# Optimization experiments

Measured on AMD Instinct MI355X. Metric: run time of the kernel, lower is better.

Reference implementation:

```python
import jax, jax.numpy as jnp
import numpy as np
from jax import lax

B, D_MODEL, T = 4, 256, 8192
D_STATE, D_CONV = 16, 4
D_INNER = 2 * D_MODEL          # expand=2.0
DT_RANK = (D_MODEL + 15) // 16 # ceil(d_model/16) = 16
EPS = 1e-5


def setup_inputs() -> dict:
    key = jax.random.key(0)
    ks = jax.random.split(key, 12)
    s = lambda k, shape, scale=0.02: (jax.random.normal(k, shape, jnp.float32) * scale)
    x = jax.random.normal(ks[0], (B, D_MODEL, T), jnp.float32)
    ln_w = jnp.ones((D_MODEL,), jnp.float32)
    ln_b = jnp.zeros((D_MODEL,), jnp.float32)
    in_proj_w = s(ks[1], (2 * D_INNER, D_MODEL))
    conv_w = s(ks[2], (D_INNER, 1, D_CONV), 0.1)
    conv_b = jnp.zeros((D_INNER,), jnp.float32)
    x_proj_w = s(ks[3], (DT_RANK + 2 * D_STATE, D_INNER))
    dt_proj_w = s(ks[4], (D_INNER, DT_RANK), 0.1)
    # bias init so softplus(dt_bias) ~ small positive dt, like mamba_ssm
    dt_proj_b = jnp.log(jnp.expm1(jax.random.uniform(ks[5], (D_INNER,), jnp.float32, 0.001, 0.1)))
    # S4D-real init: A_log = log(1..d_state) broadcast over d_inner
    A_log = jnp.log(jnp.tile(jnp.arange(1, D_STATE + 1, dtype=jnp.float32), (D_INNER, 1)))
    D = jnp.ones((D_INNER,), jnp.float32)
    out_proj_w = s(ks[6], (D_MODEL, D_INNER))
    return {"x": x, "ln_w": ln_w, "ln_b": ln_b, "in_proj_w": in_proj_w,
            "conv_w": conv_w, "conv_b": conv_b, "x_proj_w": x_proj_w,
            "dt_proj_w": dt_proj_w, "dt_proj_b": dt_proj_b, "A_log": A_log,
            "D": D, "out_proj_w": out_proj_w}


def _mamba_block(x, ln_w, ln_b, in_proj_w, conv_w, conv_b, x_proj_w,
                 dt_proj_w, dt_proj_b, A_log, D, out_proj_w):
    # x: (B, C, T)
    residual = x
    xt = jnp.transpose(x, (0, 2, 1))  # (B, T, C)
    # channel layernorm
    mu = jnp.mean(xt, axis=-1, keepdims=True)
    var = jnp.var(xt, axis=-1, keepdims=True)
    xn = (xt - mu) * lax.rsqrt(var + EPS) * ln_w + ln_b
    # in_proj -> x, z
    xz = jnp.einsum('btc,ec->bte', xn, in_proj_w)  # (B,T,2*d_inner)
    x_in, z = jnp.split(xz, 2, axis=-1)
    # causal depthwise conv over time
    xc = jnp.transpose(x_in, (0, 2, 1))  # (B, d_inner, T)
    xc = lax.conv_general_dilated(xc, conv_w, window_strides=(1,),
                                  padding=[(D_CONV - 1, 0)],
                                  dimension_numbers=('NCH', 'OIH', 'NCH'),
                                  feature_group_count=D_INNER)
    xc = xc + conv_b[None, :, None]
    u = jax.nn.silu(jnp.transpose(xc, (0, 2, 1)))  # (B,T,d_inner)
    # x_proj -> dt, B, C
    dbl = jnp.einsum('btd,ed->bte', u, x_proj_w)
    dt, Bm, Cm = jnp.split(dbl, [DT_RANK, DT_RANK + D_STATE], axis=-1)
    delta = jax.nn.softplus(jnp.einsum('btr,dr->btd', dt, dt_proj_w) + dt_proj_b)  # (B,T,d_inner)
    A = -jnp.exp(A_log)  # (d_inner, d_state)
    deltaA = jnp.exp(jnp.einsum('btd,dn->btdn', delta, A))          # (B,T,d,n)
    deltaBu = jnp.einsum('btd,btn->btdn', delta * u, Bm)            # (B,T,d,n)
    # selective scan over time
    def step(h, inp):
        dA_t, dBu_t, C_t = inp
        h = dA_t * h + dBu_t                       # (B,d,n)
        y = jnp.einsum('bdn,bn->bd', h, C_t)
        return h, y
    h0 = jnp.zeros((x.shape[0], D_INNER, D_STATE), x.dtype)
    _, ys = lax.scan(step, h0, (jnp.moveaxis(deltaA, 1, 0),
                                jnp.moveaxis(deltaBu, 1, 0),
                                jnp.moveaxis(Cm, 1, 0)))
    y = jnp.moveaxis(ys, 0, 1) + u * D             # (B,T,d_inner)
    y = y * jax.nn.silu(z)
    out = jnp.einsum('btd,cd->btc', y, out_proj_w)  # (B,T,C)
    return jnp.transpose(out, (0, 2, 1)) + residual


def reference(x, ln_w, ln_b, in_proj_w, conv_w, conv_b, x_proj_w,
              dt_proj_w, dt_proj_b, A_log, D, out_proj_w):
    return _mamba_block(x, ln_w, ln_b, in_proj_w, conv_w, conv_b, x_proj_w,
                        dt_proj_w, dt_proj_b, A_log, D, out_proj_w)
```

## Files before the change

### kernel.cpp

```cpp
#include <hip/hip_runtime.h>

typedef unsigned short u16;
typedef unsigned int u32;
typedef __bf16 bfx8 __attribute__((ext_vector_type(8)));
typedef float f32x4 __attribute__((ext_vector_type(4)));

#define Tn 8192
#define Bn 4
#define MTOT 32768
#define CH 128
#define TC 64

#define OFF_W     0ul
#define OFF_AL2   917504ul
#define OFF_XN    (1ul<<20)
#define OFF_XIN   (17ul<<20)
#define OFF_Z     (49ul<<20)
#define OFF_U     (81ul<<20)
#define OFF_DBLDT (113ul<<20)
#define OFF_BCF   (115ul<<20)
#define OFF_DELTA (119ul<<20)
#define OFF_P     (151ul<<20)
#define OFF_CC    (167ul<<20)

__device__ __forceinline__ float b2f(u16 h){ return __uint_as_float(((u32)h)<<16); }
__device__ __forceinline__ u16 f2b(float f){
  u32 u = __float_as_uint(f);
  return (u16)((u + 0x7FFFu + ((u>>16)&1u)) >> 16);
}
__device__ __forceinline__ float aexp2(float x){ float r; asm("v_exp_f32 %0, %1" : "=v"(r) : "v"(x)); return r; }
__device__ __forceinline__ float arcp (float x){ float r; asm("v_rcp_f32 %0, %1" : "=v"(r) : "v"(x)); return r; }
__device__ __forceinline__ float alog2(float x){ float r; asm("v_log_f32 %0, %1" : "=v"(r) : "v"(x)); return r; }
__device__ __forceinline__ float fsilu(float a){ return a*arcp(1.f + aexp2(-a*1.44269504f)); }
__device__ __forceinline__ float fsoftplus(float v){
  float r = 0.69314718f*alog2(1.f + aexp2(v*1.44269504f));
  return (v > 20.f) ? v : r;
}
typedef const __attribute__((address_space(1))) void* gp1_t;
typedef __attribute__((address_space(3))) void* lp3_t;
__device__ __forceinline__ void gload_lds16(const void* g, void* l){
  __builtin_amdgcn_global_load_lds((gp1_t)g, (lp3_t)l, 16, 0, 0);
}

__global__ void wconv_k(const float* __restrict__ inw, const float* __restrict__ xpw,
                        const float* __restrict__ dtw, const float* __restrict__ opw,
                        const float* __restrict__ alog, u16* __restrict__ W, float* __restrict__ aL2)
{
  int i = blockIdx.x*256 + threadIdx.x;
  if (i < 262144) { W[i] = f2b(inw[i]); return; }
  if (i < 294912) { int j = i - 262144; int r = j >> 9, k = j & 511;
    float v = (r < 16) ? xpw[r*512 + k] : ((r < 32) ? 0.f : xpw[(r-16)*512 + k]);
    W[i] = f2b(v); return; }
  if (i < 311296) { int j = i - 294912; int d = j >> 5, k = j & 31;
    W[i] = f2b((k < 16) ? dtw[d*16 + k] : 0.f); return; }
  if (i < 442368) { W[i] = f2b(opw[i - 311296]); return; }
  if (i < 450560) { int j = i - 442368; aL2[j] = -__expf(alog[j]) * 1.44269504088896f; return; }
}

__global__ __launch_bounds__(256)
void ln_k(const float* __restrict__ x, const float* __restrict__ lnw,
          const float* __restrict__ lnb, u16* __restrict__ xn)
{
  const int t0 = blockIdx.x*64, b = blockIdx.y;
  const int tid = threadIdx.x, cg = tid>>6, tl = tid&63;
  __shared__ float ps[4][64], pq[4][64], mu[64], rs[64];
  float s = 0.f, q = 0.f;
  for (int ci = 0; ci < 64; ci++){
    int c = ci*4 + cg;
    float v = x[((size_t)(b*256 + c))*Tn + t0 + tl];
    s += v; q += v*v;
  }
  ps[cg][tl] = s; pq[cg][tl] = q;
  __syncthreads();
  if (tid < 64){
    float S = ps[0][tid]+ps[1][tid]+ps[2][tid]+ps[3][tid];
    float Q = pq[0][tid]+pq[1][tid]+pq[2][tid]+pq[3][tid];
    float m = S*(1.f/256.f);
    float var = Q*(1.f/256.f) - m*m;
    mu[tid] = m; rs[tid] = rsqrtf(var + 1e-5f);
  }
  __syncthreads();
  const float w = lnw[tid&255], bb = lnb[tid&255];
  for (int t = 0; t < 64; t++){
    float v = x[((size_t)(b*256 + tid))*Tn + t0 + t];
    xn[((size_t)(b*Tn) + t0 + t)*256 + tid] = f2b((v - mu[t])*rs[t]*w + bb);
  }
}

template<int BN, int EPI>
__global__ __launch_bounds__(256)
void gemm_k(const u16* __restrict__ A, int lda,
            const u16* __restrict__ Bw, int ldb,
            u16* __restrict__ O, u16* __restrict__ O2, float* __restrict__ Of, int ldo,
            const float* __restrict__ bias, int K)
{
  constexpr int NFR = BN/32;
  __shared__ __align__(16) u16 sA[128*32];
  __shared__ __align__(16) u16 sB[BN*32];
  const int tid = threadIdx.x;
  const int m0 = blockIdx.x*128, n0 = blockIdx.y*BN;
  const int lane = tid & 63, wid = tid >> 6;
  const int wr = wid >> 1, wc = wid & 1;
  const int lr = lane & 15, g = lane >> 4;
  const f32x4 fz = {0.f,0.f,0.f,0.f};
  f32x4 acc[4][NFR];
  #pragma unroll
  for (int m=0;m<4;m++)
    #pragma unroll
    for (int n=0;n<NFR;n++) acc[m][n] = fz;
  const int nk = K >> 5;
  for (int kt = 0; kt < nk; ++kt){
    __syncthreads();
    #pragma unroll
    for (int i=0;i<2;i++){ int ci = i*256 + tid;
      gload_lds16(A + (size_t)(m0+(ci>>2))*lda + kt*32 + (ci&3)*8, sA + ci*8); }
    #pragma unroll
    for (int i=0;i<BN/64;i++){ int ci = i*256 + tid;
      gload_lds16(Bw + (size_t)(n0+(ci>>2))*ldb + kt*32 + (ci&3)*8, sB + ci*8); }
    __syncthreads();
    bfx8 af[4], bf[NFR];
    #pragma unroll
    for (int m=0;m<4;m++) af[m] = *(const bfx8*)(sA + (wr*64 + m*16 + lr)*32 + g*8);
    #pragma unroll
    for (int n=0;n<NFR;n++) bf[n] = *(const bfx8*)(sB + (wc*(BN/2) + n*16 + lr)*32 + g*8);
    #pragma unroll
    for (int m=0;m<4;m++)
      #pragma unroll
      for (int n=0;n<NFR;n++)
        acc[m][n] = __builtin_amdgcn_mfma_f32_16x16x32_bf16(af[m], bf[n], acc[m][n], 0, 0, 0);
  }
  #pragma unroll
  for (int m=0;m<4;m++)
    #pragma unroll
    for (int n=0;n<NFR;n++)
      #pragma unroll
      for (int r=0;r<4;r++){
        int row = m0 + wr*64 + m*16 + g*4 + r;
        int col = n0 + wc*(BN/2) + n*16 + lr;
        float v = acc[m][n][r];
        if (EPI == 0){
          O[(size_t)row*ldo + col] = f2b(v);
        } else if (EPI == 1){
          O[(size_t)row*ldo + col] = f2b(fsoftplus(v + bias[col]));
        } else if (EPI == 2){
          if (col < 512) O[(size_t)row*512 + col] = f2b(v);
          else           O2[(size_t)row*512 + (col-512)] = f2b(v);
        } else {
          if (col < 32) O[(size_t)row*32 + col] = f2b(v);
          else          Of[(size_t)row*32 + (col-32)] = v;
        }
      }
}

__global__ __launch_bounds__(256)
void conv_k(const u16* __restrict__ xin, const float* __restrict__ cw,
            const float* __restrict__ cb, u16* __restrict__ u)
{
  const int t0 = blockIdx.x*32, d0 = blockIdx.y*64, b = blockIdx.z;
  const int tid = threadIdx.x;
  __shared__ float sx[35][64];
  __shared__ float sw[4][64];
  { int d = tid>>2, j = tid&3; sw[j][d] = cw[(d0+d)*4 + j]; }
  for (int i=0;i<9;i++){ int f = i*256 + tid; if (f < 35*64){
      int r = f>>6, dd = f&63; int t = t0 - 3 + r;
      sx[r][dd] = (t >= 0) ? b2f(xin[((size_t)(b*Tn)+t)*512 + d0+dd]) : 0.f; } }
  __syncthreads();
  const float cbv = cb[d0 + (tid&63)];
  for (int oi=0; oi<8; oi++){
    int f = oi*256 + tid; int tr = f>>6, dd = f&63;
    float a = cbv;
    #pragma unroll
    for (int j=0;j<4;j++) a += sw[j][dd]*sx[tr+j][dd];
    u[((size_t)(b*Tn)+t0+tr)*512 + d0+dd] = f2b(fsilu(a));
  }
}

__global__ __launch_bounds__(256)
void scanA_k(const u16* __restrict__ delta, const u16* __restrict__ u,
             const float* __restrict__ bcf, const float* __restrict__ aL2,
             float* __restrict__ P, float* __restrict__ CC)
{
  const int ch = blockIdx.x, d = blockIdx.y*256 + threadIdx.x, b = blockIdx.z;
  const int t0 = ch*TC;
  float aL[16], h[16];
  #pragma unroll
  for (int i=0;i<4;i++) *(f32x4*)(aL+4*i) = *(const f32x4*)(aL2 + (size_t)d*16 + 4*i);
  #pragma unroll
  for (int n=0;n<16;n++) h[n] = 0.f;
  bool st = true;
  #pragma unroll
  for (int n=1;n<16;n++) st = st && (fabsf(aL[n] - (n+1)*aL[0]) <= 2e-4f*fabsf(aL[n]));
  const u16* dp = delta + (size_t)(b*Tn + t0)*512 + d;
  const u16* up = u     + (size_t)(b*Tn + t0)*512 + d;
  const float* bp = bcf + (size_t)(b*Tn + t0)*32;
  float sdlt = 0.f;
  const float aL0 = aL[0];
  if (st){
    for (int t=0;t<TC;t++){
      float dlt = b2f(dp[(size_t)t*512]);
      float uu  = b2f(up[(size_t)t*512]);
      float Bv[16];
      #pragma unroll
      for (int i=0;i<4;i++) *(f32x4*)(Bv+4*i) = *(const f32x4*)(bp + (size_t)t*32 + 4*i);
      float du = dlt*uu; sdlt += dlt;
      float r = aexp2(dlt*aL0);
      float r2 = r*r, e = r, f = r2;
      #pragma unroll
      for (int n=0;n<16;n+=2){
        h[n]   = fmaf(e, h[n],   du*Bv[n]);
        h[n+1] = fmaf(f, h[n+1], du*Bv[n+1]);
        e *= r2; f *= r2;
      }
    }
  } else {
    for (int t=0;t<TC;t++){
      float dlt = b2f(dp[(size_t)t*512]);
      float uu  = b2f(up[(size_t)t*512]);
      float Bv[16];
      #pragma unroll
      for (int i=0;i<4;i++) *(f32x4*)(Bv+4*i) = *(const f32x4*)(bp + (size_t)t*32 + 4*i);
      float du = dlt*uu; sdlt += dlt;
      #pragma unroll
      for (int n=0;n<16;n++)
        h[n] = fmaf(aexp2(dlt*aL[n]), h[n], du*Bv[n]);
    }
  }
  float Pq[16];
  #pragma unroll
  for (int n=0;n<16;n++) Pq[n] = aexp2(sdlt*aL[n]);
  size_t o = ((size_t)((b*CH+ch)*512 + d))<<4;
  #pragma unroll
  for (int i=0;i<4;i++){
    *(f32x4*)(P +o+4*i) = *(f32x4*)(Pq+4*i);
    *(f32x4*)(CC+o+4*i) = *(f32x4*)(h +4*i);
  }
}

__global__ __launch_bounds__(256)
void scanB_k(float* __restrict__ P, const float* __restrict__ CC)
{
  const int gid = blockIdx.x*256 + threadIdx.x;
  const int b = gid >> 11, r = gid & 2047;
  const size_t base = (size_t)(r>>2)*16 + (size_t)(r&3)*4;
  f32x4 h = {0.f,0.f,0.f,0.f};
  #pragma unroll 4
  for (int ch=0; ch<CH; ch++){
    size_t idx = ((size_t)(b*CH+ch))*8192 + base;
    f32x4 Pv = *(f32x4*)(P+idx);
    f32x4 cv = *(const f32x4*)(CC+idx);
    *(f32x4*)(P+idx) = h;
    h = Pv*h + cv;
  }
}

__global__ __launch_bounds__(256)
void scanC_k(const u16* __restrict__ delta, const u16* __restrict__ u,
             const float* __restrict__ bcf, const u16* __restrict__ z,
             const float* __restrict__ aL2, const float* __restrict__ h0,
             const float* __restrict__ Dp, u16* __restrict__ yg)
{
  const int ch = blockIdx.x, d = blockIdx.y*256 + threadIdx.x, b = blockIdx.z;
  const int t0 = ch*TC;
  float aL[16], h[16];
  #pragma unroll
  for (int i=0;i<4;i++) *(f32x4*)(aL+4*i) = *(const f32x4*)(aL2 + (size_t)d*16 + 4*i);
  size_t o = ((size_t)((b*CH+ch)*512 + d))<<4;
  #pragma unroll
  for (int i=0;i<4;i++) *(f32x4*)(h+4*i) = *(const f32x4*)(h0+o+4*i);
  bool st = true;
  #pragma unroll
  for (int n=1;n<16;n++) st = st && (fabsf(aL[n] - (n+1)*aL[0]) <= 2e-4f*fabsf(aL[n]));
  const float Dd = Dp[d];
  const float aL0 = aL[0];
  const u16* dp = delta + (size_t)(b*Tn + t0)*512 + d;
  const u16* up = u     + (size_t)(b*Tn + t0)*512 + d;
  const u16* zp = z     + (size_t)(b*Tn + t0)*512 + d;
  const float* bp = bcf + (size_t)(b*Tn + t0)*32;
  u16* yp = yg + (size_t)(b*Tn + t0)*512 + d;
  if (st){
    for (int t=0;t<TC;t++){
      float dlt = b2f(dp[(size_t)t*512]);
      float uu  = b2f(up[(size_t)t*512]);
      float zz  = b2f(zp[(size_t)t*512]);
      float Bv[16], Cv[16];
      #pragma unroll
      for (int i=0;i<4;i++){
        *(f32x4*)(Bv+4*i) = *(const f32x4*)(bp + (size_t)t*32 + 4*i);
        *(f32x4*)(Cv+4*i) = *(const f32x4*)(bp + (size_t)t*32 + 16 + 4*i);
      }
      float du = dlt*uu;
      float r = aexp2(dlt*aL0);
      float r2 = r*r, e = r, f = r2;
      float p0=0.f, p1=0.f;
      #pragma unroll
      for (int n=0;n<16;n+=2){
        h[n]   = fmaf(e, h[n],   du*Bv[n]);   p0 = fmaf(h[n],   Cv[n],   p0);
        h[n+1] = fmaf(f, h[n+1], du*Bv[n+1]); p1 = fmaf(h[n+1], Cv[n+1], p1);
        e *= r2; f *= r2;
      }
      float p = p0 + p1;
      float gy = (p + uu*Dd) * fsilu(zz);
      yp[(size_t)t*512] = f2b(gy);
    }
  } else {
    for (int t=0;t<TC;t++){
      float dlt = b2f(dp[(size_t)t*512]);
      float uu  = b2f(up[(size_t)t*512]);
      float zz  = b2f(zp[(size_t)t*512]);
      float Bv[16], Cv[16];
      #pragma unroll
      for (int i=0;i<4;i++){
        *(f32x4*)(Bv+4*i) = *(const f32x4*)(bp + (size_t)t*32 + 4*i);
        *(f32x4*)(Cv+4*i) = *(const f32x4*)(bp + (size_t)t*32 + 16 + 4*i);
      }
      float du = dlt*uu;
      float p0 = 0.f;
      #pragma unroll
      for (int n=0;n<16;n++){
        h[n] = fmaf(aexp2(dlt*aL[n]), h[n], du*Bv[n]);
        p0 = fmaf(h[n], Cv[n], p0);
      }
      float gy = (p0 + uu*Dd) * fsilu(zz);
      yp[(size_t)t*512] = f2b(gy);
    }
  }
}

__global__ __launch_bounds__(256)
void transres_k(const u16* __restrict__ yt, const float* __restrict__ x, float* __restrict__ out)
{
  const int t0 = blockIdx.x*64, c0 = blockIdx.y*64, b = blockIdx.z;
  const int tid = threadIdx.x;
  __shared__ float st[64][65];
  for (int i=0;i<16;i++){ int f=i*256+tid; int tr=f>>6, cc=f&63;
    st[tr][cc] = b2f(yt[((size_t)(b*Tn)+t0+tr)*256 + c0+cc]); }
  __syncthreads();
  for (int i=0;i<16;i++){ int f=i*256+tid; int cr=f>>6, tt=f&63;
    size_t oa = ((size_t)(b*256)+c0+cr)*Tn + t0+tt;
    out[oa] = st[tt][cr] + x[oa]; }
}

extern "C" void kernel_launch(void* const* d_in, const int* in_sizes, int n_in,
                              void* d_out, int out_size, void* d_ws, size_t ws_size,
                              hipStream_t stream)
{
  const float* x    = (const float*)d_in[0];
  const float* lnw  = (const float*)d_in[1];
  const float* lnb  = (const float*)d_in[2];
  const float* inw  = (const float*)d_in[3];
  const float* cw   = (const float*)d_in[4];
  const float* cb   = (const float*)d_in[5];
  const float* xpw  = (const float*)d_in[6];
  const float* dtw  = (const float*)d_in[7];
  const float* dtb  = (const float*)d_in[8];
  const float* alog = (const float*)d_in[9];
  const float* Dp   = (const float*)d_in[10];
  const float* opw  = (const float*)d_in[11];
  float* out = (float*)d_out;
  char* ws = (char*)d_ws;

  u16*   W     = (u16*)(ws + OFF_W);
  float* aL2   = (float*)(ws + OFF_AL2);
  u16*   xn    = (u16*)(ws + OFF_XN);
  u16*   xin   = (u16*)(ws + OFF_XIN);
  u16*   z     = (u16*)(ws + OFF_Z);
  u16*   u     = (u16*)(ws + OFF_U);
  u16*   dblDT = (u16*)(ws + OFF_DBLDT);
  float* bcf   = (float*)(ws + OFF_BCF);
  u16*   delta = (u16*)(ws + OFF_DELTA);
  float* P     = (float*)(ws + OFF_P);
  float* CC    = (float*)(ws + OFF_CC);
  u16*   yg    = xin;
  u16*   ytmp  = xn;

  wconv_k<<<1760, 256, 0, stream>>>(inw, xpw, dtw, opw, alog, W, aL2);
  ln_k<<<dim3(Tn/64, Bn), 256, 0, stream>>>(x, lnw, lnb, xn);
  gemm_k<128,2><<<dim3(MTOT/128, 8), 256, 0, stream>>>(xn, 256, W, 256, xin, z, nullptr, 512, nullptr, 256);
  conv_k<<<dim3(Tn/32, 8, Bn), 256, 0, stream>>>(xin, cw, cb, u);
  gemm_k<64,3><<<dim3(MTOT/128, 1), 256, 0, stream>>>(u, 512, W + 262144, 512, dblDT, nullptr, bcf, 32, nullptr, 512);
  gemm_k<128,1><<<dim3(MTOT/128, 4), 256, 0, stream>>>(dblDT, 32, W + 294912, 32, delta, nullptr, nullptr, 512, dtb, 32);
  scanA_k<<<dim3(CH, 2, Bn), 256, 0, stream>>>(delta, u, bcf, aL2, P, CC);
  scanB_k<<<32, 256, 0, stream>>>(P, CC);
  scanC_k<<<dim3(CH, 2, Bn), 256, 0, stream>>>(delta, u, bcf, z, aL2, P, Dp, yg);
  gemm_k<128,0><<<dim3(MTOT/128, 2), 256, 0, stream>>>(yg, 512, W + 311296, 512, ytmp, nullptr, nullptr, 256, nullptr, 512);
  transres_k<<<dim3(Tn/64, 4, Bn), 256, 0, stream>>>(ytmp, x, out);
}
```

Before: 230.3 us.

## Fuse out-proj GEMM with transpose+residual, rework scan power tree and scanB parallelism

Replaces the final out-projection GEMM plus separate transpose/residual kernel with one kernel that stages accumulators in LDS and writes the transposed output with the residual added. This removes the bf16 intermediate round trip and one launch. The scan kernels now compute the decay powers with a shallower multiply tree, use more partial dot-product accumulators, and add unroll pragmas to expose more instruction-level parallelism. scanB now uses one thread per scalar state with 4x more blocks, replacing vec4 loads. The fused epilogue's strided transposed stores and extra LDS use may lower occupancy.

```diff
diff --git a/kernel.cpp b/kernel.cpp
--- a/kernel.cpp
+++ b/kernel.cpp
@@ -138,9 +138,7 @@
         int row = m0 + wr*64 + m*16 + g*4 + r;
         int col = n0 + wc*(BN/2) + n*16 + lr;
         float v = acc[m][n][r];
-        if (EPI == 0){
-          O[(size_t)row*ldo + col] = f2b(v);
-        } else if (EPI == 1){
+        if (EPI == 1){
           O[(size_t)row*ldo + col] = f2b(fsoftplus(v + bias[col]));
         } else if (EPI == 2){
           if (col < 512) O[(size_t)row*512 + col] = f2b(v);
@@ -150,6 +148,68 @@
           else          Of[(size_t)row*32 + (col-32)] = v;
         }
       }
+}
+
+__global__ __launch_bounds__(256)
+void gemmot_k(const u16* __restrict__ A, const u16* __restrict__ Bw,
+              const float* __restrict__ x, float* __restrict__ out)
+{
+  __shared__ __align__(16) u16 sA[128*32];
+  __shared__ __align__(16) u16 sB[128*32];
+  __shared__ float st[64][129];
+  const int tid = threadIdx.x;
+  const int m0 = blockIdx.x*128, n0 = blockIdx.y*128;
+  const int lane = tid & 63, wid = tid >> 6;
+  const int wr = wid >> 1, wc = wid & 1;
+  const int lr = lane & 15, g = lane >> 4;
+  const f32x4 fz = {0.f,0.f,0.f,0.f};
+  f32x4 acc[4][4];
+  #pragma unroll
+  for (int m=0;m<4;m++)
+    #pragma unroll
+    for (int n=0;n<4;n++) acc[m][n] = fz;
+  for (int kt = 0; kt < 16; ++kt){
+    __syncthreads();
+    #pragma unroll
+    for (int i=0;i<2;i++){ int ci = i*256 + tid;
+      gload_lds16(A + (size_t)(m0+(ci>>2))*512 + kt*32 + (ci&3)*8, sA + ci*8); }
+    #pragma unroll
+    for (int i=0;i<2;i++){ int ci = i*256 + tid;
+      gload_lds16(Bw + (size_t)(n0+(ci>>2))*512 + kt*32 + (ci&3)*8, sB + ci*8); }
+    __syncthreads();
+    bfx8 af[4], bf[4];
+    #pragma unroll
+    for (int m=0;m<4;m++) af[m] = *(const bfx8*)(sA + (wr*64 + m*16 + lr)*32 + g*8);
+    #pragma unroll
+    for (int n=0;n<4;n++) bf[n] = *(const bfx8*)(sB + (wc*64 + n*16 + lr)*32 + g*8);
+    #pragma unroll
+    for (int m=0;m<4;m++)
+      #pragma unroll
+      for (int n=0;n<4;n++)
+        acc[m][n] = __builtin_amdgcn_mfma_f32_16x16x32_bf16(af[m], bf[n], acc[m][n], 0, 0, 0);
+  }
+  const int b = m0 >> 13, t0 = m0 & 8191;
+  const int tl = tid & 63, cgrp = tid >> 6;
+  for (int hf=0; hf<2; hf++){
+    __syncthreads();
+    if (wr == hf){
+      #pragma unroll
+      for (int m=0;m<4;m++)
+        #pragma unroll
+        for (int n=0;n<4;n++)
+          #pragma unroll
+          for (int r=0;r<4;r++)
+            st[m*16 + g*4 + r][wc*64 + n*16 + lr] = acc[m][n][r];
+    }
+    __syncthreads();
+    const int tg = t0 + hf*64 + tl;
+    #pragma unroll
+    for (int ci=0; ci<32; ci++){
+      int c = cgrp*32 + ci;
+      size_t oa = ((size_t)(b*256) + n0 + c)*Tn + tg;
+      out[oa] = st[tl][c] + x[oa];
+    }
+  }
 }
 
 __global__ __launch_bounds__(256)
@@ -175,6 +235,15 @@
   }
 }
 
+__device__ __forceinline__ void powtree(float r1, float* e){
+  float r2 = r1*r1;
+  float r3 = r2*r1, r4 = r2*r2;
+  float r5 = r4*r1, r6 = r4*r2, r7 = r4*r3, r8 = r4*r4;
+  e[0]=r1; e[1]=r2; e[2]=r3; e[3]=r4; e[4]=r5; e[5]=r6; e[6]=r7; e[7]=r8;
+  #pragma unroll
+  for (int k=0;k<8;k++) e[8+k] = r8*e[k];
+}
+
 __global__ __launch_bounds__(256)
 void scanA_k(const u16* __restrict__ delta, const u16* __restrict__ u,
              const float* __restrict__ bcf, const float* __restrict__ aL2,
@@ -196,6 +265,7 @@
   float sdlt = 0.f;
   const float aL0 = aL[0];
   if (st){
+    #pragma unroll 4
     for (int t=0;t<TC;t++){
       float dlt = b2f(dp[(size_t)t*512]);
       float uu  = b2f(up[(size_t)t*512]);
@@ -203,16 +273,14 @@
       #pragma unroll
       for (int i=0;i<4;i++) *(f32x4*)(Bv+4*i) = *(const f32x4*)(bp + (size_t)t*32 + 4*i);
       float du = dlt*uu; sdlt += dlt;
-      float r = aexp2(dlt*aL0);
-      float r2 = r*r, e = r, f = r2;
-      #pragma unroll
-      for (int n=0;n<16;n+=2){
-        h[n]   = fmaf(e, h[n],   du*Bv[n]);
-        h[n+1] = fmaf(f, h[n+1], du*Bv[n+1]);
-        e *= r2; f *= r2;
-      }
+      float e[16];
+      powtree(aexp2(dlt*aL0), e);
+      #pragma unroll
+      for (int n=0;n<16;n++)
+        h[n] = fmaf(e[n], h[n], du*Bv[n]);
     }
   } else {
+    #pragma unroll 2
     for (int t=0;t<TC;t++){
       float dlt = b2f(dp[(size_t)t*512]);
       float uu  = b2f(up[(size_t)t*512]);
@@ -240,16 +308,16 @@
 void scanB_k(float* __restrict__ P, const float* __restrict__ CC)
 {
   const int gid = blockIdx.x*256 + threadIdx.x;
-  const int b = gid >> 11, r = gid & 2047;
-  const size_t base = (size_t)(r>>2)*16 + (size_t)(r&3)*4;
-  f32x4 h = {0.f,0.f,0.f,0.f};
+  const int b = gid >> 13, r = gid & 8191;
+  const size_t base = (size_t)b*CH*8192 + r;
+  float h = 0.f;
   #pragma unroll 4
   for (int ch=0; ch<CH; ch++){
-    size_t idx = ((size_t)(b*CH+ch))*8192 + base;
-    f32x4 Pv = *(f32x4*)(P+idx);
-    f32x4 cv = *(const f32x4*)(CC+idx);
-    *(f32x4*)(P+idx) = h;
-    h = Pv*h + cv;
+    size_t idx = base + (size_t)ch*8192;
+    float Pv = P[idx];
+    float cv = CC[idx];
+    P[idx] = h;
+    h = fmaf(Pv, h, cv);
   }
 }
 
@@ -278,6 +346,7 @@
   const float* bp = bcf + (size_t)(b*Tn + t0)*32;
   u16* yp = yg + (size_t)(b*Tn + t0)*512 + d;
   if (st){
+    #pragma unroll 2
     for (int t=0;t<TC;t++){
       float dlt = b2f(dp[(size_t)t*512]);
       float uu  = b2f(up[(size_t)t*512]);
@@ -289,20 +358,22 @@
         *(f32x4*)(Cv+4*i) = *(const f32x4*)(bp + (size_t)t*32 + 16 + 4*i);
       }
       float du = dlt*uu;
-      float r = aexp2(dlt*aL0);
-      float r2 = r*r, e = r, f = r2;
-      float p0=0.f, p1=0.f;
-      #pragma unroll
-      for (int n=0;n<16;n+=2){
-        h[n]   = fmaf(e, h[n],   du*Bv[n]);   p0 = fmaf(h[n],   Cv[n],   p0);
-        h[n+1] = fmaf(f, h[n+1], du*Bv[n+1]); p1 = fmaf(h[n+1], Cv[n+1], p1);
-        e *= r2; f *= r2;
+      float e[16];
+      powtree(aexp2(dlt*aL0), e);
+      float p0=0.f, p1=0.f, p2=0.f, p3=0.f;
+      #pragma unroll
+      for (int n=0;n<16;n+=4){
+        h[n]   = fmaf(e[n],   h[n],   du*Bv[n]);   p0 = fmaf(h[n],   Cv[n],   p0);
+        h[n+1] = fmaf(e[n+1], h[n+1], du*Bv[n+1]); p1 = fmaf(h[n+1], Cv[n+1], p1);
+        h[n+2] = fmaf(e[n+2], h[n+2], du*Bv[n+2]); p2 = fmaf(h[n+2], Cv[n+2], p2);
+        h[n+3] = fmaf(e[n+3], h[n+3], du*Bv[n+3]); p3 = fmaf(h[n+3], Cv[n+3], p3);
       }
-      float p = p0 + p1;
+      float p = (p0+p1) + (p2+p3);
       float gy = (p + uu*Dd) * fsilu(zz);
       yp[(size_t)t*512] = f2b(gy);
     }
   } else {
+    #pragma unroll 2
     for (int t=0;t<TC;t++){
       float dlt = b2f(dp[(size_t)t*512]);
       float uu  = b2f(up[(size_t)t*512]);
@@ -324,20 +395,6 @@
       yp[(size_t)t*512] = f2b(gy);
     }
   }
-}
-
-__global__ __launch_bounds__(256)
-void transres_k(const u16* __restrict__ yt, const float* __restrict__ x, float* __restrict__ out)
-{
-  const int t0 = blockIdx.x*64, c0 = blockIdx.y*64, b = blockIdx.z;
-  const int tid = threadIdx.x;
-  __shared__ float st[64][65];
-  for (int i=0;i<16;i++){ int f=i*256+tid; int tr=f>>6, cc=f&63;
-    st[tr][cc] = b2f(yt[((size_t)(b*Tn)+t0+tr)*256 + c0+cc]); }
-  __syncthreads();
-  for (int i=0;i<16;i++){ int f=i*256+tid; int cr=f>>6, tt=f&63;
-    size_t oa = ((size_t)(b*256)+c0+cr)*Tn + t0+tt;
-    out[oa] = st[tt][cr] + x[oa]; }
 }
 
 extern "C" void kernel_launch(void* const* d_in, const int* in_sizes, int n_in,
@@ -371,17 +428,15 @@
   float* P     = (float*)(ws + OFF_P);
   float* CC    = (float*)(ws + OFF_CC);
   u16*   yg    = xin;
-  u16*   ytmp  = xn;
 
   wconv_k<<<1760, 256, 0, stream>>>(inw, xpw, dtw, opw, alog, W, aL2);
   ln_k<<<dim3(Tn/64, Bn), 256, 0, stream>>>(x, lnw, lnb, xn);
   gemm_k<128,2><<<dim3(MTOT/128, 8), 256, 0, stream>>>(xn, 256, W, 256, xin, z, nullptr, 512, nullptr, 256);
   conv_k<<<dim3(Tn/32, 8, Bn), 256, 0, stream>>>(xin, cw, cb, u);
-  gemm_k<64,3><<<dim3(MTOT/128, 1), 256, 0, stream>>>(u, 512, W + 262144, 512, dblDT, nullptr, bcf, 32, nullptr, 512);
+  gemm_k<64,3><<<dim3(MTOT/128, 1), 256, 0, stream>>>(u, 512, W + 262144, 512, dblDT, nullptr, bcf, 0, nullptr, 512);
   gemm_k<128,1><<<dim3(MTOT/128, 4), 256, 0, stream>>>(dblDT, 32, W + 294912, 32, delta, nullptr, nullptr, 512, dtb, 32);
   scanA_k<<<dim3(CH, 2, Bn), 256, 0, stream>>>(delta, u, bcf, aL2, P, CC);
-  scanB_k<<<32, 256, 0, stream>>>(P, CC);
+  scanB_k<<<128, 256, 0, stream>>>(P, CC);
   scanC_k<<<dim3(CH, 2, Bn), 256, 0, stream>>>(delta, u, bcf, z, aL2, P, Dp, yg);
-  gemm_k<128,0><<<dim3(MTOT/128, 2), 256, 0, stream>>>(yg, 512, W + 311296, 512, ytmp, nullptr, nullptr, 256, nullptr, 512);
-  transres_k<<<dim3(Tn/64, 4, Bn), 256, 0, stream>>>(ytmp, x, out);
-}
+  gemmot_k<<<dim3(MTOT/128, 2), 256, 0, stream>>>(yg, W + 311296, x, out);
+}
```

Result: faster. 224.0 us (-2.7%).
